# Kernel tuning notes

Measured on AMD Instinct MI355X. Metric: run time of the kernel, lower is better.

The kernel has to match this reference:

```python
import jax, jax.numpy as jnp
import numpy as np

T, D, H, E, K = 8192, 1024, 4096, 8, 2


def setup_inputs() -> dict:
    key = jax.random.key(0)
    ks = jax.random.split(key, 6)
    s_in = 1.0 / np.sqrt(D)
    s_hid = 1.0 / np.sqrt(H)
    return {
        "hidden_states": jax.random.normal(ks[0], (T, D), dtype=jnp.float32),
        "router_w": jax.random.normal(ks[1], (D, E), dtype=jnp.float32) * s_in,
        "expert_w1": jax.random.normal(ks[2], (E, D, H), dtype=jnp.float32) * s_in,
        "expert_w2": jax.random.normal(ks[3], (E, H, D), dtype=jnp.float32) * s_hid,
        "shared_w1": jax.random.normal(ks[4], (D, H), dtype=jnp.float32) * s_in,
        "shared_w2": jax.random.normal(ks[5], (H, D), dtype=jnp.float32) * s_hid,
    }


def reference(hidden_states, router_w, expert_w1, expert_w2, shared_w1, shared_w2):
    x = hidden_states  # [T, D]
    # --- router: softmax over experts, keep top-k, renormalize ---
    probs = jax.nn.softmax(x @ router_w, axis=-1)            # [T, E]
    top_v, top_i = jax.lax.top_k(probs, K)                   # [T, K]
    top_v = top_v / jnp.sum(top_v, axis=-1, keepdims=True)
    # dense combine weights [T, E]; zero for non-selected experts
    comb = jnp.zeros((x.shape[0], E), x.dtype).at[
        jnp.arange(x.shape[0])[:, None], top_i].set(top_v)
    # --- routed experts (dense reference for grouped GEMM) ---
    h = jax.nn.silu(jnp.einsum('td,edh->eth', x, expert_w1))  # [E, T, H]
    eo = jnp.einsum('eth,ehd->etd', h, expert_w2)             # [E, T, D]
    routed = jnp.einsum('te,etd->td', comb, eo)               # [T, D]
    # --- shared expert, always active ---
    shared = jax.nn.silu(x @ shared_w1) @ shared_w2           # [T, D]
    return routed + shared
```

## Files before the change

### kernel.cpp

```cpp
#include <hip/hip_runtime.h>
#include <hip/hip_bf16.h>
#include <stdint.h>

typedef unsigned short u16;
typedef __attribute__((ext_vector_type(8))) short bf16x8;
typedef __attribute__((ext_vector_type(4))) float f32x4;

constexpr int T_ = 8192;
constexpr int D_ = 1024;
constexpr int H_ = 4096;
constexpr int E_ = 8;
constexpr int MAXROWS = 25600;
constexpr int NTILES  = 200;

__device__ __forceinline__ unsigned int f2bf_bits(float f) {
  unsigned int u = __float_as_uint(f);
  return (u + 0x7fffu + ((u >> 16) & 1u)) >> 16;
}

__device__ __forceinline__ void load_lds16(const void* g, void* s) {
  __builtin_amdgcn_global_load_lds(
      (const __attribute__((address_space(1))) unsigned int*)g,
      (__attribute__((address_space(3))) unsigned int*)s, 16, 0, 0);
}

__global__ __launch_bounds__(256) void router_kernel(
    const float* __restrict__ x, const float* __restrict__ rw,
    int* __restrict__ counts, int* __restrict__ tok2, float* __restrict__ wgt2) {
  __shared__ float rw_s[E_ * D_];
  __shared__ int c_s[E_];
  const int tid = threadIdx.x;
  if (tid < E_) c_s[tid] = 0;
  for (int f = tid; f < 2048; f += 256) {
    int d = f >> 1, p = f & 1;
    float4 v = *(const float4*)(rw + d * 8 + p * 4);
    rw_s[(p * 4 + 0) * D_ + d] = v.x;
    rw_s[(p * 4 + 1) * D_ + d] = v.y;
    rw_s[(p * 4 + 2) * D_ + d] = v.z;
    rw_s[(p * 4 + 3) * D_ + d] = v.w;
  }
  __syncthreads();
  const int wid = tid >> 6, lane = tid & 63;
  for (int ti = 0; ti < 16; ++ti) {
    const int t = blockIdx.x * 64 + wid * 16 + ti;
    const float* xr = x + (long)t * D_;
    float acc[E_] = {0.f, 0.f, 0.f, 0.f, 0.f, 0.f, 0.f, 0.f};
    for (int j = 0; j < 16; ++j) {
      const int d = lane + 64 * j;
      const float xv = xr[d];
#pragma unroll
      for (int e = 0; e < E_; ++e) acc[e] += xv * rw_s[e * D_ + d];
    }
#pragma unroll
    for (int off = 32; off >= 1; off >>= 1) {
#pragma unroll
      for (int e = 0; e < E_; ++e) acc[e] += __shfl_xor(acc[e], off, 64);
    }
    if (lane == 0) {
      int i0 = 0; float l0 = acc[0];
#pragma unroll
      for (int e = 1; e < E_; ++e) if (acc[e] > l0) { l0 = acc[e]; i0 = e; }
      int i1 = -1; float l1 = -3.4e38f;
#pragma unroll
      for (int e = 0; e < E_; ++e) if (e != i0 && acc[e] > l1) { l1 = acc[e]; i1 = e; }
      const float r = __expf(l1 - l0);
      const float inv = 1.f / (1.f + r);
      tok2[2 * t] = i0; tok2[2 * t + 1] = i1;
      wgt2[2 * t] = inv; wgt2[2 * t + 1] = r * inv;
      atomicAdd(&c_s[i0], 1); atomicAdd(&c_s[i1], 1);
    }
  }
  __syncthreads();
  if (tid < E_) atomicAdd(&counts[tid], c_s[tid]);
}

__global__ void scan_kernel(const int* __restrict__ counts, int* __restrict__ offs,
                            int* __restrict__ tile_expert, int* __restrict__ rowtok) {
  __shared__ int so[10];
  const int tid = threadIdx.x;
  if (tid == 0) {
    int o = 0;
    for (int e = 0; e < E_; ++e) { so[e] = o; o += ((counts[e] + 127) >> 7) << 7; }
    so[8] = o;
    o += T_;
    so[9] = o;
    for (int i = 0; i < 10; ++i) offs[i] = so[i];
  }
  __syncthreads();
  for (int i = tid; i < NTILES; i += 256) {
    const int row = i << 7;
    int e = 8;
    if (row < so[8]) {
      e = 7;
      for (int k = 0; k < 7; ++k) if (row < so[k + 1]) { e = k; break; }
    }
    tile_expert[i] = e;
  }
  for (int r = tid; r < MAXROWS; r += 256) rowtok[r] = 0;
}

__global__ __launch_bounds__(256) void assign_kernel(
    const int* __restrict__ tok2, const int* __restrict__ offs,
    int* __restrict__ cursors, int* __restrict__ rowtok, int* __restrict__ pos2) {
  __shared__ int lcnt[E_], lbase[E_];
  const int tid = threadIdx.x;
  if (tid < E_) lcnt[tid] = 0;
  __syncthreads();
  const int t = blockIdx.x * 256 + tid;
  const int e0 = tok2[2 * t], e1 = tok2[2 * t + 1];
  const int s0 = atomicAdd(&lcnt[e0], 1);
  const int s1 = atomicAdd(&lcnt[e1], 1);
  __syncthreads();
  if (tid < E_) lbase[tid] = offs[tid] + atomicAdd(&cursors[tid], lcnt[tid]);
  __syncthreads();
  const int p0 = lbase[e0] + s0, p1 = lbase[e1] + s1;
  rowtok[p0] = t; rowtok[p1] = t;
  pos2[2 * t] = p0; pos2[2 * t + 1] = p1;
  rowtok[offs[8] + t] = t;
}

__global__ __launch_bounds__(256) void cvt_x_kernel(const float* __restrict__ x,
                                                    u16* __restrict__ xb) {
  const long i = ((long)blockIdx.x * 256 + threadIdx.x) * 4;
  const float4 v = *(const float4*)(x + i);
  ushort4 o;
  o.x = (u16)f2bf_bits(v.x); o.y = (u16)f2bf_bits(v.y);
  o.z = (u16)f2bf_bits(v.z); o.w = (u16)f2bf_bits(v.w);
  *(ushort4*)(xb + i) = o;
}

__global__ __launch_bounds__(256) void transpose_cvt_kernel(
    const float* __restrict__ src8, const float* __restrict__ srcShared,
    u16* __restrict__ dst, int R, int C) {
  __shared__ float tile[64][65];
  const long stride = (long)R * C;
  const float* src = (blockIdx.z < 8) ? src8 + (long)blockIdx.z * stride : srcShared;
  u16* d = dst + (long)blockIdx.z * stride;
  const int tid = threadIdx.x;
  const int r0 = blockIdx.y * 64, c0 = blockIdx.x * 64;
  const int lr = tid >> 4, lc4 = tid & 15;
#pragma unroll
  for (int p = 0; p < 4; ++p) {
    const float4 v = *(const float4*)(src + (long)(r0 + lr + 16 * p) * C + c0 + lc4 * 4);
    tile[lr + 16 * p][lc4 * 4 + 0] = v.x;
    tile[lr + 16 * p][lc4 * 4 + 1] = v.y;
    tile[lr + 16 * p][lc4 * 4 + 2] = v.z;
    tile[lr + 16 * p][lc4 * 4 + 3] = v.w;
  }
  __syncthreads();
#pragma unroll
  for (int p = 0; p < 4; ++p) {
    const int rr = lr + 16 * p;
    ushort4 o;
    o.x = (u16)f2bf_bits(tile[lc4 * 4 + 0][rr]);
    o.y = (u16)f2bf_bits(tile[lc4 * 4 + 1][rr]);
    o.z = (u16)f2bf_bits(tile[lc4 * 4 + 2][rr]);
    o.w = (u16)f2bf_bits(tile[lc4 * 4 + 3][rr]);
    *(ushort4*)(d + (long)(c0 + rr) * R + r0 + lc4 * 4) = o;
  }
}

template <bool G1, int CHM>
__global__ __launch_bounds__(256) void moe_gemm(
    const u16* __restrict__ A, const u16* __restrict__ Bt, void* __restrict__ C,
    const int* __restrict__ rowtok, const int* __restrict__ tile_expert) {
  constexpr int K = G1 ? 1024 : 4096;
  constexpr int N = G1 ? 4096 : 1024;
  constexpr int NT = N / 128;
  __shared__ u16 As[2 * 4096];
  __shared__ u16 Bs[2 * 4096];

  const int tid = threadIdx.x;
  int mt, nt;
  {
    const int bid = blockIdx.x;
    const int cb = CHM * NT;
    const int chunk = bid / cb;
    const int mt0 = chunk * CHM;
    const int m = min(CHM, NTILES - mt0);
    const int rem = bid - chunk * cb;
    mt = mt0 + rem % m;
    nt = rem / m;
  }
  const int e = tile_expert[mt];

  const int sr = tid >> 2;
  const int sc = (tid & 3) << 3;

  long aoff0, aoff1;
  if constexpr (G1) {
    aoff0 = (long)rowtok[mt * 128 + sr] * K;
    aoff1 = (long)rowtok[mt * 128 + 64 + sr] * K;
  } else {
    aoff0 = (long)(mt * 128 + sr) * K;
    aoff1 = (long)(mt * 128 + 64 + sr) * K;
  }
  const u16* pa0 = A + aoff0 + sc;
  const u16* pa1 = A + aoff1 + sc;
  const u16* pb0 = Bt + (long)e * N * K + (long)(nt * 128 + sr) * K + sc;
  const u16* pb1 = pb0 + (long)64 * K;

  u16* sA0[2] = {As + tid * 8, As + 4096 + tid * 8};
  u16* sA1[2] = {As + 2048 + tid * 8, As + 4096 + 2048 + tid * 8};
  u16* sB0[2] = {Bs + tid * 8, Bs + 4096 + tid * 8};
  u16* sB1[2] = {Bs + 2048 + tid * 8, Bs + 4096 + 2048 + tid * 8};

  const int lane = tid & 63;
  const int wid = tid >> 6;
  const int wm = (wid >> 1) * 64;
  const int wn = (wid & 1) * 64;
  const int lr = lane & 15;
  const int quad = lane >> 4;

  f32x4 acc[4][4] = {};

  load_lds16(pa0, sA0[0]);
  load_lds16(pa1, sA1[0]);
  load_lds16(pb0, sB0[0]);
  load_lds16(pb1, sB1[0]);

#pragma unroll 1
  for (int k0 = 0; k0 < K; k0 += 64) {
    __syncthreads();
    if (k0 + 32 < K) {
      load_lds16(pa0 + k0 + 32, sA0[1]);
      load_lds16(pa1 + k0 + 32, sA1[1]);
      load_lds16(pb0 + k0 + 32, sB0[1]);
      load_lds16(pb1 + k0 + 32, sB1[1]);
    }
    {
      bf16x8 af[4], bfv[4];
#pragma unroll
      for (int i = 0; i < 4; ++i)
        af[i] = *(const bf16x8*)(As + (wm + i * 16 + lr) * 32 + quad * 8);
#pragma unroll
      for (int j = 0; j < 4; ++j)
        bfv[j] = *(const bf16x8*)(Bs + (wn + j * 16 + lr) * 32 + quad * 8);
#pragma unroll
      for (int i = 0; i < 4; ++i)
#pragma unroll
        for (int j = 0; j < 4; ++j)
          acc[i][j] = __builtin_amdgcn_mfma_f32_16x16x32_bf16(af[i], bfv[j], acc[i][j], 0, 0, 0);
    }
    __syncthreads();
    if (k0 + 64 < K) {
      load_lds16(pa0 + k0 + 64, sA0[0]);
      load_lds16(pa1 + k0 + 64, sA1[0]);
      load_lds16(pb0 + k0 + 64, sB0[0]);
      load_lds16(pb1 + k0 + 64, sB1[0]);
    }
    {
      bf16x8 af[4], bfv[4];
#pragma unroll
      for (int i = 0; i < 4; ++i)
        af[i] = *(const bf16x8*)(As + 4096 + (wm + i * 16 + lr) * 32 + quad * 8);
#pragma unroll
      for (int j = 0; j < 4; ++j)
        bfv[j] = *(const bf16x8*)(Bs + 4096 + (wn + j * 16 + lr) * 32 + quad * 8);
#pragma unroll
      for (int i = 0; i < 4; ++i)
#pragma unroll
        for (int j = 0; j < 4; ++j)
          acc[i][j] = __builtin_amdgcn_mfma_f32_16x16x32_bf16(af[i], bfv[j], acc[i][j], 0, 0, 0);
    }
  }

  const int rbase = mt * 128 + wm + quad * 4;
  if constexpr (G1) {
    u16* Hout = (u16*)C;
#pragma unroll
    for (int i = 0; i < 4; ++i) {
#pragma unroll
      for (int j = 0; j < 4; ++j) {
#pragma unroll
        for (int r = 0; r < 4; ++r) {
          float v = acc[i][j][r];
          v = v / (1.f + __expf(-v));
          unsigned int u = f2bf_bits(v);
          unsigned int other = (unsigned int)__shfl_xor((int)u, 1, 64);
          if (!(lane & 1)) {
            const unsigned int w = (u & 0xffffu) | (other << 16);
            const long row = rbase + i * 16 + r;
            const int col = nt * 128 + wn + j * 16 + lr;
            *(unsigned int*)(Hout + row * N + col) = w;
          }
        }
      }
    }
  } else {
    float* O = (float*)C;
#pragma unroll
    for (int i = 0; i < 4; ++i)
#pragma unroll
      for (int j = 0; j < 4; ++j)
#pragma unroll
        for (int r = 0; r < 4; ++r) {
          const long row = rbase + i * 16 + r;
          const int col = nt * 128 + wn + j * 16 + lr;
          O[row * N + col] = acc[i][j][r];
        }
  }
}

__global__ __launch_bounds__(256) void combine_kernel(
    const float* __restrict__ eo, const int* __restrict__ pos2,
    const float* __restrict__ wgt2, const int* __restrict__ offs,
    float* __restrict__ out) {
  const int t = blockIdx.x, tid = threadIdx.x;
  const int p0 = pos2[2 * t], p1 = pos2[2 * t + 1];
  const float w0 = wgt2[2 * t], w1 = wgt2[2 * t + 1];
  const int ps = offs[8] + t;
  const long c = (long)tid * 4;
  const float4 a = *(const float4*)(eo + (long)p0 * D_ + c);
  const float4 b = *(const float4*)(eo + (long)p1 * D_ + c);
  const float4 s = *(const float4*)(eo + (long)ps * D_ + c);
  float4 o;
  o.x = w0 * a.x + w1 * b.x + s.x;
  o.y = w0 * a.y + w1 * b.y + s.y;
  o.z = w0 * a.z + w1 * b.z + s.z;
  o.w = w0 * a.w + w1 * b.w + s.w;
  *(float4*)(out + (long)t * D_ + c) = o;
}

extern "C" void kernel_launch(void* const* d_in, const int* in_sizes, int n_in,
                              void* d_out, int out_size, void* d_ws, size_t ws_size,
                              hipStream_t stream) {
  const float* x   = (const float*)d_in[0];
  const float* rw  = (const float*)d_in[1];
  const float* w1  = (const float*)d_in[2];
  const float* w2  = (const float*)d_in[3];
  const float* sw1 = (const float*)d_in[4];
  const float* sw2 = (const float*)d_in[5];
  float* out = (float*)d_out;

  char* ws = (char*)d_ws;
  int*   counts      = (int*)(ws + 0);
  int*   cursors     = (int*)(ws + 64);
  int*   offs        = (int*)(ws + 128);
  int*   tile_expert = (int*)(ws + 192);
  int*   tok2        = (int*)(ws + 4096);
  float* wgt2        = (float*)(ws + 4096 + 65536);
  int*   pos2        = (int*)(ws + 4096 + 131072);
  int*   rowtok      = (int*)(ws + 4096 + 196608);

  size_t off = 1u << 20;
  u16* xb  = (u16*)(ws + off); off += (size_t)T_ * D_ * 2;
  u16* w1t = (u16*)(ws + off); off += (size_t)9 * H_ * D_ * 2;
  u16* w2t = (u16*)(ws + off); off += (size_t)9 * D_ * H_ * 2;
  u16* h   = (u16*)(ws + off); off += (size_t)MAXROWS * H_ * 2;
  float* eo = (float*)(ws + off); off += (size_t)MAXROWS * D_ * 4;

  hipMemsetAsync(ws, 0, 256, stream);
  router_kernel<<<128, 256, 0, stream>>>(x, rw, counts, tok2, wgt2);
  scan_kernel<<<1, 256, 0, stream>>>(counts, offs, tile_expert, rowtok);
  assign_kernel<<<32, 256, 0, stream>>>(tok2, offs, cursors, rowtok, pos2);
  cvt_x_kernel<<<T_ * D_ / 1024, 256, 0, stream>>>(x, xb);
  transpose_cvt_kernel<<<dim3(H_ / 64, D_ / 64, 9), 256, 0, stream>>>(w1, sw1, w1t, D_, H_);
  transpose_cvt_kernel<<<dim3(D_ / 64, H_ / 64, 9), 256, 0, stream>>>(w2, sw2, w2t, H_, D_);
  moe_gemm<true, 24><<<NTILES * (H_ / 128), 256, 0, stream>>>(xb, w1t, h, rowtok, tile_expert);
  moe_gemm<false, 64><<<NTILES * (D_ / 128), 256, 0, stream>>>(h, w2t, eo, rowtok, tile_expert);
  combine_kernel<<<T_, 256, 0, stream>>>(eo, pos2, wgt2, offs, out);
}
```

Before: 1.082 ms.

## Triple-buffer LDS staging with swizzled layout and single barrier per k-step

```diff
diff --git a/kernel.cpp b/kernel.cpp
--- a/kernel.cpp
+++ b/kernel.cpp
@@ -167,8 +167,9 @@
   constexpr int K = G1 ? 1024 : 4096;
   constexpr int N = G1 ? 4096 : 1024;
   constexpr int NT = N / 128;
-  __shared__ u16 As[2 * 4096];
-  __shared__ u16 Bs[2 * 4096];
+  constexpr int NIT = K / 32;
+  __shared__ u16 As[3 * 4096];
+  __shared__ u16 Bs[3 * 4096];
 
   const int tid = threadIdx.x;
   int mt, nt;
@@ -185,7 +186,7 @@
   const int e = tile_expert[mt];
 
   const int sr = tid >> 2;
-  const int sc = (tid & 3) << 3;
+  const int sc = (((tid & 3) ^ ((sr >> 1) & 3)) << 3);
 
   long aoff0, aoff1;
   if constexpr (G1) {
@@ -200,70 +201,61 @@
   const u16* pb0 = Bt + (long)e * N * K + (long)(nt * 128 + sr) * K + sc;
   const u16* pb1 = pb0 + (long)64 * K;
 
-  u16* sA0[2] = {As + tid * 8, As + 4096 + tid * 8};
-  u16* sA1[2] = {As + 2048 + tid * 8, As + 4096 + 2048 + tid * 8};
-  u16* sB0[2] = {Bs + tid * 8, Bs + 4096 + tid * 8};
-  u16* sB1[2] = {Bs + 2048 + tid * 8, Bs + 4096 + 2048 + tid * 8};
-
   const int lane = tid & 63;
   const int wid = tid >> 6;
   const int wm = (wid >> 1) * 64;
   const int wn = (wid & 1) * 64;
   const int lr = lane & 15;
   const int quad = lane >> 4;
+  const int cA = ((quad ^ ((lr >> 1) & 3)) << 3);
 
   f32x4 acc[4][4] = {};
 
-  load_lds16(pa0, sA0[0]);
-  load_lds16(pa1, sA1[0]);
-  load_lds16(pb0, sB0[0]);
-  load_lds16(pb1, sB1[0]);
-
+  auto stage = [&](int b, int koff) {
+    u16* a_d = As + b * 4096 + tid * 8;
+    u16* b_d = Bs + b * 4096 + tid * 8;
+    load_lds16(pa0 + koff, a_d);
+    load_lds16(pa1 + koff, a_d + 2048);
+    load_lds16(pb0 + koff, b_d);
+    load_lds16(pb1 + koff, b_d + 2048);
+  };
+  auto compute = [&](int b) {
+    const u16* a_s = As + b * 4096;
+    const u16* b_s = Bs + b * 4096;
+    bf16x8 af[4], bfv[4];
+#pragma unroll
+    for (int i = 0; i < 4; ++i)
+      af[i] = *(const bf16x8*)(a_s + (wm + i * 16 + lr) * 32 + cA);
+#pragma unroll
+    for (int j2 = 0; j2 < 4; ++j2)
+      bfv[j2] = *(const bf16x8*)(b_s + (wn + j2 * 16 + lr) * 32 + cA);
+    __builtin_amdgcn_s_setprio(1);
+#pragma unroll
+    for (int i = 0; i < 4; ++i)
+#pragma unroll
+      for (int j2 = 0; j2 < 4; ++j2)
+        acc[i][j2] =
+            __builtin_amdgcn_mfma_f32_16x16x32_bf16(af[i], bfv[j2], acc[i][j2], 0, 0, 0);
+    __builtin_amdgcn_s_setprio(0);
+  };
+
+  stage(0, 0);
+  asm volatile("" ::: "memory");
+  stage(1, 32);
+
+  int cur = 0;
 #pragma unroll 1
-  for (int k0 = 0; k0 < K; k0 += 64) {
-    __syncthreads();
-    if (k0 + 32 < K) {
-      load_lds16(pa0 + k0 + 32, sA0[1]);
-      load_lds16(pa1 + k0 + 32, sA1[1]);
-      load_lds16(pb0 + k0 + 32, sB0[1]);
-      load_lds16(pb1 + k0 + 32, sB1[1]);
-    }
-    {
-      bf16x8 af[4], bfv[4];
-#pragma unroll
-      for (int i = 0; i < 4; ++i)
-        af[i] = *(const bf16x8*)(As + (wm + i * 16 + lr) * 32 + quad * 8);
-#pragma unroll
-      for (int j = 0; j < 4; ++j)
-        bfv[j] = *(const bf16x8*)(Bs + (wn + j * 16 + lr) * 32 + quad * 8);
-#pragma unroll
-      for (int i = 0; i < 4; ++i)
-#pragma unroll
-        for (int j = 0; j < 4; ++j)
-          acc[i][j] = __builtin_amdgcn_mfma_f32_16x16x32_bf16(af[i], bfv[j], acc[i][j], 0, 0, 0);
-    }
-    __syncthreads();
-    if (k0 + 64 < K) {
-      load_lds16(pa0 + k0 + 64, sA0[0]);
-      load_lds16(pa1 + k0 + 64, sA1[0]);
-      load_lds16(pb0 + k0 + 64, sB0[0]);
-      load_lds16(pb1 + k0 + 64, sB1[0]);
-    }
-    {
-      bf16x8 af[4], bfv[4];
-#pragma unroll
-      for (int i = 0; i < 4; ++i)
-        af[i] = *(const bf16x8*)(As + 4096 + (wm + i * 16 + lr) * 32 + quad * 8);
-#pragma unroll
-      for (int j = 0; j < 4; ++j)
-        bfv[j] = *(const bf16x8*)(Bs + 4096 + (wn + j * 16 + lr) * 32 + quad * 8);
-#pragma unroll
-      for (int i = 0; i < 4; ++i)
-#pragma unroll
-        for (int j = 0; j < 4; ++j)
-          acc[i][j] = __builtin_amdgcn_mfma_f32_16x16x32_bf16(af[i], bfv[j], acc[i][j], 0, 0, 0);
-    }
-  }
+  for (int j = 0; j < NIT - 1; ++j) {
+    asm volatile("s_waitcnt vmcnt(4)\n\ts_barrier" ::: "memory");
+    if (j + 2 < NIT) {
+      const int nb = (cur == 0) ? 2 : cur - 1;
+      stage(nb, (j + 2) * 32);
+    }
+    compute(cur);
+    cur = (cur == 2) ? 0 : cur + 1;
+  }
+  asm volatile("s_waitcnt vmcnt(0)\n\ts_barrier" ::: "memory");
+  compute(cur);
 
   const int rbase = mt * 128 + wm + quad * 4;
   if constexpr (G1) {
```

After: 1.043 ms. -3.6%, faster.
